# Kernel tuning notes

Hardware: AMD Instinct MI355X
Metric: run time of the kernel (lower is better)

Reference implementation:

```python
import jax, jax.numpy as jnp
import numpy as np

T, IN, H, OUT = 4096, 2048, 2048, 1


def setup_inputs() -> dict:
    key = jax.random.key(0)
    ks = jax.random.split(key, 7)
    s = 0.02  # small init scale to keep gates in a sane range
    return {
        "x": jax.random.normal(ks[0], (T, 1, IN), dtype=jnp.float32),
        "W_ih": s * jax.random.normal(ks[1], (4 * H, IN), dtype=jnp.float32),
        "W_hh": s * jax.random.normal(ks[2], (4 * H, H), dtype=jnp.float32),
        "b_ih": s * jax.random.normal(ks[3], (4 * H,), dtype=jnp.float32),
        "b_hh": s * jax.random.normal(ks[4], (4 * H,), dtype=jnp.float32),
        "W_out": s * jax.random.normal(ks[5], (OUT, H), dtype=jnp.float32),
        "b_out": s * jax.random.normal(ks[6], (OUT,), dtype=jnp.float32),
    }


def reference(x, W_ih, W_hh, b_ih, b_hh, W_out, b_out):
    # Faithful LSTMCell loop (PyTorch gate order i, f, g, o) + per-step Linear.
    hidden = W_hh.shape[1]

    def step(carry, x_t):  # x_t: [1, IN]
        h, c = carry
        gates = x_t @ W_ih.T + b_ih + h @ W_hh.T + b_hh  # [1, 4H]
        i, f, g, o = jnp.split(gates, 4, axis=-1)
        i = jax.nn.sigmoid(i)
        f = jax.nn.sigmoid(f)
        g = jnp.tanh(g)
        o = jax.nn.sigmoid(o)
        c = f * c + i * g
        h = o * jnp.tanh(c)
        y = (h @ W_out.T + b_out)[0, 0]  # scalar, output_size == 1
        return (h, c), y

    h0 = jnp.zeros((1, hidden), dtype=x.dtype)
    c0 = jnp.zeros((1, hidden), dtype=x.dtype)
    _, res = jax.lax.scan(step, (h0, c0), x)
    return res  # [T]
```

## Files before the change

kernel.cpp:

```cpp
#include <hip/hip_runtime.h>

#define T_STEPS 4096
#define HD 2048
#define G4 8192
#define NWG 256
#define NTH 1024
#define HSENT 0xFF80u
#define HSENT2 0xFF80FF80u

#define HB_OFF  131072
#define P_OFF   (131072 + 8192)
#define SMEM_BYTES (131072 + 8192 + 2048)

typedef __attribute__((ext_vector_type(8))) short bf16x8;
typedef __attribute__((ext_vector_type(4))) float f32x4;
typedef __attribute__((ext_vector_type(8))) unsigned short u16x8;

static __device__ __forceinline__ unsigned short f2bf(float f){
  union { float f; unsigned int u; } v; v.f = f;
  unsigned int r = (v.u + 0x7fffu + ((v.u >> 16) & 1u)) >> 16;
  return (unsigned short)r;
}
static __device__ __forceinline__ float bf2f(unsigned short s){
  union { unsigned int u; float f; } v; v.u = ((unsigned int)s) << 16;
  return v.f;
}

static __device__ __forceinline__ unsigned int ld1_uc(const unsigned int* p){
  unsigned int r;
  asm volatile("global_load_dword %0, %1, off sc0 sc1\n\ts_waitcnt vmcnt(0)"
               : "=v"(r) : "v"(p) : "memory");
  return r;
}
static __device__ __forceinline__ void st2_uc(unsigned short* p, unsigned int v){
  asm volatile("global_store_short %0, %1, off sc0 sc1" :: "v"(p), "v"(v) : "memory");
}

__global__ void init_kernel(const float* __restrict__ b_ih, const float* __restrict__ b_hh,
                            float* __restrict__ bias, unsigned int* __restrict__ Hb32){
  int i = blockIdx.x*blockDim.x + threadIdx.x;
  int stride = gridDim.x*blockDim.x;
  const int HB_U32 = (T_STEPS+1)*HD/2;
  const int NTOT = G4 + HB_U32;
  for (int idx = i; idx < NTOT; idx += stride){
    if (idx < G4) bias[idx] = b_ih[idx] + b_hh[idx];
    else {
      int j = idx - G4;
      Hb32[j] = (j < HD/2) ? 0u : HSENT2;
    }
  }
}

__global__ __launch_bounds__(256) void gemm_xp(const float* __restrict__ X,
                                               const float* __restrict__ W,
                                               const float* __restrict__ bias,
                                               unsigned short* __restrict__ XP){
  __shared__ __align__(16) unsigned short As[128][40];
  __shared__ __align__(16) unsigned short Bs[128][40];
  const int tid = threadIdx.x;
  const int bx = blockIdx.x & 63;
  const int by = blockIdx.x >> 6;
  const int row0 = by*128, col0 = bx*128;
  const int l = tid & 63, w = tid >> 6;
  const int wrow = (w>>1)*64, wcol = (w&1)*64;
  const int lr = l & 15, lk = l >> 4;

  f32x4 acc[4][4];
  #pragma unroll
  for (int mi=0; mi<4; mi++)
    #pragma unroll
    for (int ni=0; ni<4; ni++)
      acc[mi][ni] = (f32x4){0.f,0.f,0.f,0.f};

  const int sr = tid >> 1;
  const int sh = (tid & 1) * 16;
  const float* xb = X + (size_t)(row0+sr)*2048 + sh;
  const float* wb = W + (size_t)(col0+sr)*2048 + sh;

  for (int k0 = 0; k0 < 2048; k0 += 32){
    __syncthreads();
    u16x8 va[2], vb[2];
    #pragma unroll
    for (int q=0; q<2; q++){
      float4 u = *(const float4*)(xb + k0 + q*8);
      float4 v = *(const float4*)(xb + k0 + q*8 + 4);
      u16x8 t;
      t[0]=f2bf(u.x); t[1]=f2bf(u.y); t[2]=f2bf(u.z); t[3]=f2bf(u.w);
      t[4]=f2bf(v.x); t[5]=f2bf(v.y); t[6]=f2bf(v.z); t[7]=f2bf(v.w);
      va[q]=t;
      float4 p = *(const float4*)(wb + k0 + q*8);
      float4 r = *(const float4*)(wb + k0 + q*8 + 4);
      u16x8 s;
      s[0]=f2bf(p.x); s[1]=f2bf(p.y); s[2]=f2bf(p.z); s[3]=f2bf(p.w);
      s[4]=f2bf(r.x); s[5]=f2bf(r.y); s[6]=f2bf(r.z); s[7]=f2bf(r.w);
      vb[q]=s;
    }
    *(u16x8*)&As[sr][sh]   = va[0];
    *(u16x8*)&As[sr][sh+8] = va[1];
    *(u16x8*)&Bs[sr][sh]   = vb[0];
    *(u16x8*)&Bs[sr][sh+8] = vb[1];
    __syncthreads();

    bf16x8 af[4], bfr[4];
    #pragma unroll
    for (int mi=0; mi<4; mi++) af[mi]  = *(const bf16x8*)&As[wrow+mi*16+lr][lk*8];
    #pragma unroll
    for (int ni=0; ni<4; ni++) bfr[ni] = *(const bf16x8*)&Bs[wcol+ni*16+lr][lk*8];
    #pragma unroll
    for (int mi=0; mi<4; mi++)
      #pragma unroll
      for (int ni=0; ni<4; ni++)
        acc[mi][ni] = __builtin_amdgcn_mfma_f32_16x16x32_bf16(af[mi], bfr[ni], acc[mi][ni], 0,0,0);
  }

  #pragma unroll
  for (int ni=0; ni<4; ni++){
    const int jc = col0 + wcol + ni*16 + lr;
    const float bv = bias[jc];
    #pragma unroll
    for (int mi=0; mi<4; mi++){
      const int tr0 = row0 + wrow + mi*16 + lk*4;
      #pragma unroll
      for (int r=0; r<4; r++)
        XP[(size_t)(tr0+r)*G4 + jc] = f2bf(acc[mi][ni][r] + bv);
    }
  }
}

__global__ __launch_bounds__(NTH, 4) void recur(const unsigned short* __restrict__ XP,
                                                const float* __restrict__ Whh,
                                                unsigned short* __restrict__ Hbuf){
  extern __shared__ char smem[];
  float* part = (float*)(smem + P_OFF);
  const int g = blockIdx.x;
  const int tid = threadIdx.x;
  const int l = tid & 63, w = tid >> 6;

  #pragma unroll
  for (int n=0; n<2; n++)
    #pragma unroll
    for (int kt=0; kt<4; kt++){
      const int rr = n*16 + (l & 15);
      const size_t jrow = (size_t)(rr>>3)*HD + (size_t)g*8 + (rr&7);
      const int k = w*128 + kt*32 + (l>>4)*8;
      const float* wp = Whh + jrow*HD + k;
      float4 fa = *(const float4*)wp;
      float4 fb = *(const float4*)(wp + 4);
      uint4 pk;
      pk.x = ((unsigned)f2bf(fa.y)<<16) | f2bf(fa.x);
      pk.y = ((unsigned)f2bf(fa.w)<<16) | f2bf(fa.z);
      pk.z = ((unsigned)f2bf(fb.y)<<16) | f2bf(fb.x);
      pk.w = ((unsigned)f2bf(fb.w)<<16) | f2bf(fb.z);
      *(uint4*)(smem + (size_t)(((w*8 + n*4 + kt)*64 + l)*16)) = pk;
    }
  __syncthreads();

  float c_reg = 0.f;

  for (int t=0; t<T_STEPS; ++t){
    float xpv0=0.f, xpv1=0.f, xpv2=0.f, xpv3=0.f;
    if (tid < 8){
      const unsigned short* xp = XP + (size_t)t*G4 + (size_t)g*8 + tid;
      xpv0 = bf2f(xp[0]);
      xpv1 = bf2f(xp[HD]);
      xpv2 = bf2f(xp[2*HD]);
      xpv3 = bf2f(xp[3*HD]);
    }
    bf16x8 bfr0[4], bfr1[4];
    #pragma unroll
    for (int kt=0; kt<4; kt++){
      bfr0[kt] = *(const bf16x8*)(smem + (size_t)(((w*8 +      kt)*64 + l)*16));
      bfr1[kt] = *(const bf16x8*)(smem + (size_t)(((w*8 + 4 + kt)*64 + l)*16));
    }

    unsigned int hv;
    {
      const unsigned int* hp = (const unsigned int*)(Hbuf + (size_t)t*HD) + tid;
      do { hv = ld1_uc(hp); }
      while ((hv & 0xFFFFu) == HSENT || (hv >> 16) == HSENT);
    }
    unsigned int* hdst = (unsigned int*)(smem + HB_OFF + (t&1)*4096);
    hdst[tid] = hv;
    __syncthreads();

    const char* hb = smem + HB_OFF + (t&1)*4096;
    bf16x8 af[4];
    #pragma unroll
    for (int kt=0; kt<4; kt++)
      af[kt] = *(const bf16x8*)(hb + (w*256 + kt*64 + (l>>4)*16));

    f32x4 acc0 = (f32x4){0.f,0.f,0.f,0.f};
    f32x4 acc1 = (f32x4){0.f,0.f,0.f,0.f};
    #pragma unroll
    for (int kt=0; kt<4; kt++){
      acc0 = __builtin_amdgcn_mfma_f32_16x16x32_bf16(af[kt], bfr0[kt], acc0, 0,0,0);
      acc1 = __builtin_amdgcn_mfma_f32_16x16x32_bf16(af[kt], bfr1[kt], acc1, 0,0,0);
    }
    if (l < 16){
      part[w*32 + l]      = acc0[0];
      part[w*32 + 16 + l] = acc1[0];
    }
    __syncthreads();

    if (w == 0 && l < 32){
      float tot = 0.f;
      #pragma unroll
      for (int q=0; q<16; q++) tot += part[q*32 + l];
      float fg = __shfl_down(tot, 8, 64);
      float gg = __shfl_down(tot, 16, 64);
      float og = __shfl_down(tot, 24, 64);
      if (l < 8){
        float ipre = tot + xpv0;
        float fpre = fg  + xpv1;
        float gpre = gg  + xpv2;
        float opre = og  + xpv3;
        float iv = 1.f/(1.f + __expf(-ipre));
        float fv = 1.f/(1.f + __expf(-fpre));
        float e2 = __expf(-2.f*gpre);
        float gv = (1.f - e2)/(1.f + e2);
        float ov = 1.f/(1.f + __expf(-opre));
        c_reg = fv*c_reg + iv*gv;
        float e2c = __expf(-2.f*c_reg);
        float th = (1.f - e2c)/(1.f + e2c);
        st2_uc(Hbuf + (size_t)(t+1)*HD + (size_t)g*8 + l, (unsigned int)f2bf(ov*th));
      }
    }
  }
}

__global__ __launch_bounds__(256) void out_gemv(const unsigned short* __restrict__ Hbuf,
                                                const float* __restrict__ Wout,
                                                const float* __restrict__ bout,
                                                float* __restrict__ y){
  const int t = blockIdx.x;
  const int tid = threadIdx.x;
  u16x8 hv = *(const u16x8*)(Hbuf + (size_t)(t+1)*HD + tid*8);
  float4 w0 = *(const float4*)(Wout + tid*8);
  float4 w1 = *(const float4*)(Wout + tid*8 + 4);
  float s = bf2f(hv[0])*w0.x + bf2f(hv[1])*w0.y + bf2f(hv[2])*w0.z + bf2f(hv[3])*w0.w
          + bf2f(hv[4])*w1.x + bf2f(hv[5])*w1.y + bf2f(hv[6])*w1.z + bf2f(hv[7])*w1.w;
  #pragma unroll
  for (int off=32; off; off>>=1) s += __shfl_xor(s, off, 64);
  __shared__ float ps[4];
  if ((tid & 63) == 0) ps[tid>>6] = s;
  __syncthreads();
  if (tid == 0) y[t] = ps[0]+ps[1]+ps[2]+ps[3] + bout[0];
}

extern "C" void kernel_launch(void* const* d_in, const int* in_sizes, int n_in,
                              void* d_out, int out_size, void* d_ws, size_t ws_size,
                              hipStream_t stream) {
  const float* x    = (const float*)d_in[0];
  const float* Wih  = (const float*)d_in[1];
  const float* Whh  = (const float*)d_in[2];
  const float* b_ih = (const float*)d_in[3];
  const float* b_hh = (const float*)d_in[4];
  const float* Wout = (const float*)d_in[5];
  const float* bout = (const float*)d_in[6];
  float* y = (float*)d_out;

  char* ws = (char*)d_ws;
  unsigned short* XP   = (unsigned short*)(ws);
  unsigned short* Hbuf = (unsigned short*)(ws + 67108864);
  float* bias          = (float*)(ws + 83890176);

  init_kernel<<<2048, 256, 0, stream>>>(b_ih, b_hh, bias, (unsigned int*)Hbuf);
  gemm_xp<<<2048, 256, 0, stream>>>(x, Wih, bias, XP);

  hipFuncSetAttribute((const void*)recur,
                      hipFuncAttributeMaxDynamicSharedMemorySize, SMEM_BYTES);
  void* args[] = {(void*)&XP, (void*)&Whh, (void*)&Hbuf};
  hipLaunchCooperativeKernel((void*)recur, dim3(NWG), dim3(NTH), args,
                             SMEM_BYTES, stream);

  out_gemv<<<T_STEPS, 256, 0, stream>>>(Hbuf, Wout, bout, y);
}
```

Before: 10.75 ms.

## Halve recurrence workgroup width and pack hidden-state polling and stores

The recurrent kernel now runs 8 waves instead of 16 per workgroup. Each wave covers twice the K range with 8 MFMA steps, so the partial-sum reduction and each per-step barrier involve fewer waves. Polling of the previous hidden state uses one dwordx2 uncached load per thread, and the shared hidden buffer is no longer double-buffered. The eight new bf16 outputs are gathered with lane shuffles and written as a single dwordx4 uncached store instead of eight short stores. In exchange, each wave does a longer serial MFMA chain and holds more fragment registers, and there is less parallelism per step.

After: 11.28 ms. 1.05x slower.

```diff
diff --git a/kernel.cpp b/kernel.cpp
--- a/kernel.cpp
+++ b/kernel.cpp
@@ -4,17 +4,19 @@
 #define HD 2048
 #define G4 8192
 #define NWG 256
-#define NTH 1024
+#define NTH 512
 #define HSENT 0xFF80u
 #define HSENT2 0xFF80FF80u
 
 #define HB_OFF  131072
-#define P_OFF   (131072 + 8192)
-#define SMEM_BYTES (131072 + 8192 + 2048)
+#define P_OFF   (131072 + 4096)
+#define SMEM_BYTES (131072 + 4096 + 1024)
 
 typedef __attribute__((ext_vector_type(8))) short bf16x8;
 typedef __attribute__((ext_vector_type(4))) float f32x4;
 typedef __attribute__((ext_vector_type(8))) unsigned short u16x8;
+typedef __attribute__((ext_vector_type(2))) unsigned int u32x2;
+typedef __attribute__((ext_vector_type(4))) unsigned int u32x4;
 
 static __device__ __forceinline__ unsigned short f2bf(float f){
   union { float f; unsigned int u; } v; v.f = f;
@@ -26,14 +28,14 @@
   return v.f;
 }
 
-static __device__ __forceinline__ unsigned int ld1_uc(const unsigned int* p){
-  unsigned int r;
-  asm volatile("global_load_dword %0, %1, off sc0 sc1\n\ts_waitcnt vmcnt(0)"
+static __device__ __forceinline__ u32x2 ld2_uc(const unsigned int* p){
+  u32x2 r;
+  asm volatile("global_load_dwordx2 %0, %1, off sc0 sc1\n\ts_waitcnt vmcnt(0)"
                : "=v"(r) : "v"(p) : "memory");
   return r;
 }
-static __device__ __forceinline__ void st2_uc(unsigned short* p, unsigned int v){
-  asm volatile("global_store_short %0, %1, off sc0 sc1" :: "v"(p), "v"(v) : "memory");
+static __device__ __forceinline__ void st4_uc(unsigned int* p, u32x4 v){
+  asm volatile("global_store_dwordx4 %0, %1, off sc0 sc1" :: "v"(p), "v"(v) : "memory");
 }
 
 __global__ void init_kernel(const float* __restrict__ b_ih, const float* __restrict__ b_hh,
@@ -127,11 +129,12 @@
   }
 }
 
-__global__ __launch_bounds__(NTH, 4) void recur(const unsigned short* __restrict__ XP,
+__global__ __launch_bounds__(NTH, 1) void recur(const unsigned short* __restrict__ XP,
                                                 const float* __restrict__ Whh,
                                                 unsigned short* __restrict__ Hbuf){
   extern __shared__ char smem[];
   float* part = (float*)(smem + P_OFF);
+  char*  hb   = smem + HB_OFF;
   const int g = blockIdx.x;
   const int tid = threadIdx.x;
   const int l = tid & 63, w = tid >> 6;
@@ -139,10 +142,10 @@
   #pragma unroll
   for (int n=0; n<2; n++)
     #pragma unroll
-    for (int kt=0; kt<4; kt++){
+    for (int kt=0; kt<8; kt++){
       const int rr = n*16 + (l & 15);
       const size_t jrow = (size_t)(rr>>3)*HD + (size_t)g*8 + (rr&7);
-      const int k = w*128 + kt*32 + (l>>4)*8;
+      const int k = w*256 + kt*32 + (l>>4)*8;
       const float* wp = Whh + jrow*HD + k;
       float4 fa = *(const float4*)wp;
       float4 fb = *(const float4*)(wp + 4);
@@ -151,7 +154,7 @@
       pk.y = ((unsigned)f2bf(fa.w)<<16) | f2bf(fa.z);
       pk.z = ((unsigned)f2bf(fb.y)<<16) | f2bf(fb.x);
       pk.w = ((unsigned)f2bf(fb.w)<<16) | f2bf(fb.z);
-      *(uint4*)(smem + (size_t)(((w*8 + n*4 + kt)*64 + l)*16)) = pk;
+      *(uint4*)(smem + (size_t)(((w*16 + n*8 + kt)*64 + l)*16)) = pk;
     }
   __syncthreads();
 
@@ -166,33 +169,32 @@
       xpv2 = bf2f(xp[2*HD]);
       xpv3 = bf2f(xp[3*HD]);
     }
-    bf16x8 bfr0[4], bfr1[4];
-    #pragma unroll
-    for (int kt=0; kt<4; kt++){
-      bfr0[kt] = *(const bf16x8*)(smem + (size_t)(((w*8 +      kt)*64 + l)*16));
-      bfr1[kt] = *(const bf16x8*)(smem + (size_t)(((w*8 + 4 + kt)*64 + l)*16));
-    }
-
-    unsigned int hv;
+    bf16x8 bfr0[8], bfr1[8];
+    #pragma unroll
+    for (int kt=0; kt<8; kt++){
+      bfr0[kt] = *(const bf16x8*)(smem + (size_t)(((w*16 +     kt)*64 + l)*16));
+      bfr1[kt] = *(const bf16x8*)(smem + (size_t)(((w*16 + 8 + kt)*64 + l)*16));
+    }
+
+    u32x2 hv;
     {
-      const unsigned int* hp = (const unsigned int*)(Hbuf + (size_t)t*HD) + tid;
-      do { hv = ld1_uc(hp); }
-      while ((hv & 0xFFFFu) == HSENT || (hv >> 16) == HSENT);
-    }
-    unsigned int* hdst = (unsigned int*)(smem + HB_OFF + (t&1)*4096);
-    hdst[tid] = hv;
-    __syncthreads();
-
-    const char* hb = smem + HB_OFF + (t&1)*4096;
-    bf16x8 af[4];
-    #pragma unroll
-    for (int kt=0; kt<4; kt++)
-      af[kt] = *(const bf16x8*)(hb + (w*256 + kt*64 + (l>>4)*16));
+      const unsigned int* hp = (const unsigned int*)(Hbuf + (size_t)t*HD) + tid*2;
+      do { hv = ld2_uc(hp); }
+      while ((hv[0] & 0xFFFFu) == HSENT || (hv[0] >> 16) == HSENT ||
+             (hv[1] & 0xFFFFu) == HSENT || (hv[1] >> 16) == HSENT);
+    }
+    *(u32x2*)(hb + tid*8) = hv;
+    __syncthreads();
+
+    bf16x8 af[8];
+    #pragma unroll
+    for (int kt=0; kt<8; kt++)
+      af[kt] = *(const bf16x8*)(hb + (w*512 + kt*64 + (l>>4)*16));
 
     f32x4 acc0 = (f32x4){0.f,0.f,0.f,0.f};
     f32x4 acc1 = (f32x4){0.f,0.f,0.f,0.f};
     #pragma unroll
-    for (int kt=0; kt<4; kt++){
+    for (int kt=0; kt<8; kt++){
       acc0 = __builtin_amdgcn_mfma_f32_16x16x32_bf16(af[kt], bfr0[kt], acc0, 0,0,0);
       acc1 = __builtin_amdgcn_mfma_f32_16x16x32_bf16(af[kt], bfr1[kt], acc1, 0,0,0);
     }
@@ -205,7 +207,7 @@
     if (w == 0 && l < 32){
       float tot = 0.f;
       #pragma unroll
-      for (int q=0; q<16; q++) tot += part[q*32 + l];
+      for (int q=0; q<8; q++) tot += part[q*32 + l];
       float fg = __shfl_down(tot, 8, 64);
       float gg = __shfl_down(tot, 16, 64);
       float og = __shfl_down(tot, 24, 64);
@@ -222,7 +224,16 @@
         c_reg = fv*c_reg + iv*gv;
         float e2c = __expf(-2.f*c_reg);
         float th = (1.f - e2c)/(1.f + e2c);
-        st2_uc(Hbuf + (size_t)(t+1)*HD + (size_t)g*8 + l, (unsigned int)f2bf(ov*th));
+        unsigned v = f2bf(ov*th);
+        unsigned p1 = (unsigned)__shfl_xor((int)v, 1, 64);
+        unsigned d01 = (v & 0xFFFFu) | (p1 << 16);
+        unsigned d23 = (unsigned)__shfl_xor((int)d01, 2, 64);
+        unsigned d45 = (unsigned)__shfl_xor((int)d01, 4, 64);
+        unsigned d67 = (unsigned)__shfl_xor((int)d23, 4, 64);
+        if (l == 0){
+          u32x4 pk = (u32x4){d01, d23, d45, d67};
+          st4_uc((unsigned int*)(Hbuf + (size_t)(t+1)*HD + (size_t)g*8), pk);
+        }
       }
     }
   }
```

## Halve recurrence block size, poll h via async global-to-LDS loads, prefetch XP

Applied to the files above, without the earlier changes.

The recurrence kernel now uses 512 threads per workgroup, so each wave covers twice the K range (8 MFMA k-steps instead of 4). Polling for the previous hidden state switches from per-thread uncached dword loads plus a full barrier to per-wave global_load_lds polling with sentinel checks done in LDS. That removes one __syncthreads per step. The gate activations are computed in parallel across 32 lanes using one combined sigmoid/tanh formula. The next step's XP value is prefetched after the h store, and the partial-sum buffer is double-buffered and transposed for vector reads. The custom inline-asm polling loop depends on subtle vmcnt ordering and on each wave seeing only its own slice of h.

Result: slower. 11.36 ms (+5.7%).

```diff
diff --git a/kernel.cpp b/kernel.cpp
--- a/kernel.cpp
+++ b/kernel.cpp
@@ -4,8 +4,7 @@
 #define HD 2048
 #define G4 8192
 #define NWG 256
-#define NTH 1024
-#define HSENT 0xFF80u
+#define NTH 512
 #define HSENT2 0xFF80FF80u
 
 #define HB_OFF  131072
@@ -25,15 +24,56 @@
   union { unsigned int u; float f; } v; v.u = ((unsigned int)s) << 16;
   return v.f;
 }
-
-static __device__ __forceinline__ unsigned int ld1_uc(const unsigned int* p){
-  unsigned int r;
-  asm volatile("global_load_dword %0, %1, off sc0 sc1\n\ts_waitcnt vmcnt(0)"
-               : "=v"(r) : "v"(p) : "memory");
-  return r;
-}
 static __device__ __forceinline__ void st2_uc(unsigned short* p, unsigned int v){
   asm volatile("global_store_short %0, %1, off sc0 sc1" :: "v"(p), "v"(v) : "memory");
+}
+
+static __device__ __forceinline__ void poll_span(const unsigned int* ga, const unsigned int* gb,
+                                                 unsigned la, unsigned lb, unsigned chk){
+  unsigned t0, t1;
+  asm volatile(
+    "s_waitcnt vmcnt(0)\n\t"
+    "s_mov_b32 m0, %[la]\n\t"
+    "global_load_lds_dword %[ga], off sc0 sc1\n\t"
+    "s_mov_b32 m0, %[lb]\n\t"
+    "global_load_lds_dword %[gb], off sc0 sc1\n\t"
+    "s_sleep 2\n\t"
+    "s_mov_b32 m0, %[la]\n\t"
+    "global_load_lds_dword %[ga], off sc0 sc1\n\t"
+    "s_mov_b32 m0, %[lb]\n\t"
+    "global_load_lds_dword %[gb], off sc0 sc1\n\t"
+    "s_sleep 2\n\t"
+    "s_mov_b32 m0, %[la]\n\t"
+    "global_load_lds_dword %[ga], off sc0 sc1\n\t"
+    "s_mov_b32 m0, %[lb]\n\t"
+    "global_load_lds_dword %[gb], off sc0 sc1\n\t"
+    "s_sleep 2\n\t"
+    "s_mov_b32 m0, %[la]\n\t"
+    "global_load_lds_dword %[ga], off sc0 sc1\n\t"
+    "s_mov_b32 m0, %[lb]\n\t"
+    "global_load_lds_dword %[gb], off sc0 sc1\n\t"
+    "s_mov_b32 m0, -1\n\t"
+    "Lpoll%=:\n\t"
+    "s_waitcnt vmcnt(6)\n\t"
+    "ds_read_b32 %[t0], %[chk]\n\t"
+    "ds_read_b32 %[t1], %[chk] offset:256\n\t"
+    "s_waitcnt lgkmcnt(0)\n\t"
+    "v_xor_b32 %[t0], 0xff80ff80, %[t0]\n\t"
+    "v_xor_b32 %[t1], 0xff80ff80, %[t1]\n\t"
+    "v_min_u32 %[t0], %[t0], %[t1]\n\t"
+    "v_cmp_eq_u32 vcc, 0, %[t0]\n\t"
+    "s_cbranch_vccz Ldone%=\n\t"
+    "s_mov_b32 m0, %[la]\n\t"
+    "global_load_lds_dword %[ga], off sc0 sc1\n\t"
+    "s_mov_b32 m0, %[lb]\n\t"
+    "global_load_lds_dword %[gb], off sc0 sc1\n\t"
+    "s_mov_b32 m0, -1\n\t"
+    "s_sleep 2\n\t"
+    "s_branch Lpoll%=\n\t"
+    "Ldone%=:\n\t"
+    : [t0]"=&v"(t0), [t1]"=&v"(t1)
+    : [ga]"v"(ga), [gb]"v"(gb), [la]"s"(la), [lb]"s"(lb), [chk]"v"(chk)
+    : "vcc", "memory");
 }
 
 __global__ void init_kernel(const float* __restrict__ b_ih, const float* __restrict__ b_hh,
@@ -127,11 +167,10 @@
   }
 }
 
-__global__ __launch_bounds__(NTH, 4) void recur(const unsigned short* __restrict__ XP,
+__global__ __launch_bounds__(NTH, 1) void recur(const unsigned short* __restrict__ XP,
                                                 const float* __restrict__ Whh,
                                                 unsigned short* __restrict__ Hbuf){
   extern __shared__ char smem[];
-  float* part = (float*)(smem + P_OFF);
   const int g = blockIdx.x;
   const int tid = threadIdx.x;
   const int l = tid & 63, w = tid >> 6;
@@ -139,10 +178,10 @@
   #pragma unroll
   for (int n=0; n<2; n++)
     #pragma unroll
-    for (int kt=0; kt<4; kt++){
+    for (int kt=0; kt<8; kt++){
       const int rr = n*16 + (l & 15);
       const size_t jrow = (size_t)(rr>>3)*HD + (size_t)g*8 + (rr&7);
-      const int k = w*128 + kt*32 + (l>>4)*8;
+      const int k = w*256 + kt*32 + (l>>4)*8;
       const float* wp = Whh + jrow*HD + k;
       float4 fa = *(const float4*)wp;
       float4 fb = *(const float4*)(wp + 4);
@@ -151,78 +190,74 @@
       pk.y = ((unsigned)f2bf(fa.w)<<16) | f2bf(fa.z);
       pk.z = ((unsigned)f2bf(fb.y)<<16) | f2bf(fb.x);
       pk.w = ((unsigned)f2bf(fb.w)<<16) | f2bf(fb.z);
-      *(uint4*)(smem + (size_t)(((w*8 + n*4 + kt)*64 + l)*16)) = pk;
+      *(uint4*)(smem + (size_t)(((w*16 + n*8 + kt)*64 + l)*16)) = pk;
     }
   __syncthreads();
 
   float c_reg = 0.f;
+  float xpv = 0.f;
+  if (w == 0 && l < 32)
+    xpv = bf2f(XP[(size_t)(l>>3)*HD + (size_t)g*8 + (l&7)]);
 
   for (int t=0; t<T_STEPS; ++t){
-    float xpv0=0.f, xpv1=0.f, xpv2=0.f, xpv3=0.f;
-    if (tid < 8){
-      const unsigned short* xp = XP + (size_t)t*G4 + (size_t)g*8 + tid;
-      xpv0 = bf2f(xp[0]);
-      xpv1 = bf2f(xp[HD]);
-      xpv2 = bf2f(xp[2*HD]);
-      xpv3 = bf2f(xp[3*HD]);
-    }
-    bf16x8 bfr0[4], bfr1[4];
-    #pragma unroll
-    for (int kt=0; kt<4; kt++){
-      bfr0[kt] = *(const bf16x8*)(smem + (size_t)(((w*8 +      kt)*64 + l)*16));
-      bfr1[kt] = *(const bf16x8*)(smem + (size_t)(((w*8 + 4 + kt)*64 + l)*16));
-    }
-
-    unsigned int hv;
+    const int par = t & 1;
     {
-      const unsigned int* hp = (const unsigned int*)(Hbuf + (size_t)t*HD) + tid;
-      do { hv = ld1_uc(hp); }
-      while ((hv & 0xFFFFu) == HSENT || (hv >> 16) == HSENT);
-    }
-    unsigned int* hdst = (unsigned int*)(smem + HB_OFF + (t&1)*4096);
-    hdst[tid] = hv;
-    __syncthreads();
-
-    const char* hb = smem + HB_OFF + (t&1)*4096;
-    bf16x8 af[4];
-    #pragma unroll
-    for (int kt=0; kt<4; kt++)
-      af[kt] = *(const bf16x8*)(hb + (w*256 + kt*64 + (l>>4)*16));
+      const unsigned int* hrow = (const unsigned int*)(Hbuf + (size_t)t*HD);
+      const unsigned int* ga = hrow + w*128 + l;
+      const unsigned int* gb = ga + 64;
+      unsigned la = (unsigned)__builtin_amdgcn_readfirstlane(HB_OFF + par*4096 + w*512);
+      unsigned lb = la + 256;
+      unsigned chk = la + l*4;
+      poll_span(ga, gb, la, lb, chk);
+    }
+    const char* hb = smem + HB_OFF + par*4096 + w*512;
+
+    bf16x8 af[8];
+    #pragma unroll
+    for (int kt=0; kt<8; kt++)
+      af[kt] = *(const bf16x8*)(hb + kt*64 + (l>>4)*16);
 
     f32x4 acc0 = (f32x4){0.f,0.f,0.f,0.f};
     f32x4 acc1 = (f32x4){0.f,0.f,0.f,0.f};
     #pragma unroll
-    for (int kt=0; kt<4; kt++){
-      acc0 = __builtin_amdgcn_mfma_f32_16x16x32_bf16(af[kt], bfr0[kt], acc0, 0,0,0);
-      acc1 = __builtin_amdgcn_mfma_f32_16x16x32_bf16(af[kt], bfr1[kt], acc1, 0,0,0);
-    }
+    for (int kt=0; kt<8; kt++){
+      bf16x8 b0 = *(const bf16x8*)(smem + (size_t)(((w*16 +     kt)*64 + l)*16));
+      bf16x8 b1 = *(const bf16x8*)(smem + (size_t)(((w*16 + 8 + kt)*64 + l)*16));
+      acc0 = __builtin_amdgcn_mfma_f32_16x16x32_bf16(af[kt], b0, acc0, 0,0,0);
+      acc1 = __builtin_amdgcn_mfma_f32_16x16x32_bf16(af[kt], b1, acc1, 0,0,0);
+    }
+    float* part = (float*)(smem + P_OFF + par*1024);
     if (l < 16){
-      part[w*32 + l]      = acc0[0];
-      part[w*32 + 16 + l] = acc1[0];
+      part[l*8 + w]      = acc0[0];
+      part[(16+l)*8 + w] = acc1[0];
     }
     __syncthreads();
 
-    if (w == 0 && l < 32){
-      float tot = 0.f;
-      #pragma unroll
-      for (int q=0; q<16; q++) tot += part[q*32 + l];
-      float fg = __shfl_down(tot, 8, 64);
-      float gg = __shfl_down(tot, 16, 64);
-      float og = __shfl_down(tot, 24, 64);
+    if (w == 0){
+      __builtin_amdgcn_s_setprio(1);
+      float act = 0.f;
+      if (l < 32){
+        float4 pa = *(const float4*)(part + l*8);
+        float4 pb = *(const float4*)(part + l*8 + 4);
+        float tot = ((pa.x+pa.y)+(pa.z+pa.w)) + ((pb.x+pb.y)+(pb.z+pb.w)) + xpv;
+        const bool isg = ((l>>3) == 2);
+        float z = __expf(isg ? -2.f*tot : -tot);
+        float s = 1.f/(1.f + z);
+        act = isg ? 2.f*s - 1.f : s;
+      }
+      float fv = __shfl_down(act, 8, 64);
+      float gv = __shfl_down(act, 16, 64);
+      float ov = __shfl_down(act, 24, 64);
       if (l < 8){
-        float ipre = tot + xpv0;
-        float fpre = fg  + xpv1;
-        float gpre = gg  + xpv2;
-        float opre = og  + xpv3;
-        float iv = 1.f/(1.f + __expf(-ipre));
-        float fv = 1.f/(1.f + __expf(-fpre));
-        float e2 = __expf(-2.f*gpre);
-        float gv = (1.f - e2)/(1.f + e2);
-        float ov = 1.f/(1.f + __expf(-opre));
-        c_reg = fv*c_reg + iv*gv;
+        c_reg = fv*c_reg + act*gv;
         float e2c = __expf(-2.f*c_reg);
         float th = (1.f - e2c)/(1.f + e2c);
-        st2_uc(Hbuf + (size_t)(t+1)*HD + (size_t)g*8 + l, (unsigned int)f2bf(ov*th));
+        st2_uc(Hbuf + (size_t)(t+1)*HD + (size_t)g*8 + l, (unsigned)f2bf(ov*th));
+      }
+      __builtin_amdgcn_s_setprio(0);
+      if (l < 32){
+        const int tn = (t+1 < T_STEPS) ? t+1 : t;
+        xpv = bf2f(XP[(size_t)tn*G4 + (size_t)(l>>3)*HD + (size_t)g*8 + (l&7)]);
       }
     }
   }
```
